# Kernel tuning notes

Hardware: AMD Instinct MI355X
Metric: run time of the kernel (lower is better)

## Reference

```python
import jax, jax.numpy as jnp
import numpy as np

B, C, H, W = 32, 48, 64, 128
K = 5  # conv kernel size (1x5 / 5x1)


def _conv1d(x, w, b):
    # x: [B, C, L]; w: [O, I, K]; b: [O]. 'same' conv (pad 2) along L.
    y = jax.lax.conv_general_dilated(x, w, window_strides=(1,), padding=[(2, 2)],
                                     dimension_numbers=("NCH", "OIH", "NCH"))
    return y + b[None, :, None]


def setup_inputs() -> dict:
    key = jax.random.key(0)
    ks = jax.random.split(key, 7)
    s = 0.02  # small init so the 64/128-step linear recurrences stay bounded
    return {
        "x": jax.random.normal(ks[0], (B, C, H, W), dtype=jnp.float32),
        "down_w": jax.random.normal(ks[1], (C, C, K), dtype=jnp.float32) * s,
        "down_b": jax.random.normal(ks[2], (C,), dtype=jnp.float32) * s,
        "right_w": jax.random.normal(ks[3], (C, C, K), dtype=jnp.float32) * s,
        "right_b": jax.random.normal(ks[4], (C,), dtype=jnp.float32) * s,
        "left_w": jax.random.normal(ks[5], (C, C, K), dtype=jnp.float32) * s,
        "left_b": jax.random.normal(ks[6], (C,), dtype=jnp.float32) * s,
    }


def reference(x, down_w, down_b, right_w, right_b, left_w, left_b):
    Bb, Cc, Hh, Ww = x.shape

    def step(w, b):
        def f(carry, inp):
            nxt = inp + _conv1d(carry, w, b)
            return nxt, nxt
        return f

    # --- down pass: d[0]=x[0]; d[t]=x[t]+down_conv(d[t-1]) ---
    xs = jnp.moveaxis(x, 2, 0)                       # [H, B, C, W]
    d0 = xs[0]
    _, d_rest = jax.lax.scan(step(down_w, down_b), d0, xs[1:])
    D = jnp.concatenate([d0[None], d_rest], 0)       # [H, B, C, W]

    # --- up pass: faithfully uses down_conv (source quirk) with index H-3-t
    # u[0]=D[H-1]; u[k]=D[H-2-k]+down_conv(u[k-1]), k=1..H-1 (H-2-k=-1 -> D[H-1])
    seq = jnp.concatenate([D[Hh - 3::-1], D[Hh - 1:Hh]], 0)  # [H-1, B, C, W]
    u0 = D[Hh - 1]
    _, u_rest = jax.lax.scan(step(down_w, down_b), u0, seq)
    U = jnp.concatenate([u0[None], u_rest], 0)[::-1]  # U[i] = u[H-1-i]

    # --- right pass over width: r[0]=U[...,0]; r[t]=U[...,t]+right_conv(r[t-1]) ---
    ws = jnp.moveaxis(jnp.moveaxis(U, 0, 2), 3, 0)   # [W, B, C, H]
    r0 = ws[0]
    _, r_rest = jax.lax.scan(step(right_w, right_b), r0, ws[1:])
    R = jnp.concatenate([r0[None], r_rest], 0)       # [W, B, C, H]

    # --- left pass (reverse): l[0]=R[W-1]; l[k]=R[W-1-k]+left_conv(l[k-1]) ---
    l0 = R[Ww - 1]
    _, l_rest = jax.lax.scan(step(left_w, left_b), l0, R[Ww - 2::-1])
    L = jnp.concatenate([l0[None], l_rest], 0)[::-1]  # [W, B, C, H]

    return jnp.moveaxis(L, 0, 3)                     # [B, C, H, W]
```

## Files before the change

### kernel.cpp

```cpp
#include <hip/hip_runtime.h>
#include <hip/hip_bf16.h>

#define B_ 32
#define C_ 48
#define H_ 64
#define W_ 128
#define K_ 5
#define SLAB (C_*H_*W_)
#define RS 72
#define ROWS 132
#define KB 10
#define WC (W_*C_)
#define HC (H_*C_)

typedef __attribute__((ext_vector_type(8))) short short8;
typedef __attribute__((ext_vector_type(4))) float f32x4;

__device__ __forceinline__ void lbar() {
  asm volatile("s_waitcnt lgkmcnt(0)\n\ts_barrier" ::: "memory");
}

__device__ __forceinline__ unsigned short f2bf(float f) {
  union { float f; unsigned u; } v; v.f = f;
  unsigned r = v.u + 0x7fffu + ((v.u >> 16) & 1u);
  return (unsigned short)(r >> 16);
}

__device__ __forceinline__ unsigned pk2(float a, float b) {
  union { __hip_bfloat162 h; unsigned u; } z;
  z.h = __float22bfloat162_rn(float2{a, b});
  return z.u;
}

__device__ __forceinline__ void load_wA(const float* __restrict__ wgt,
                                        const float* __restrict__ bias,
                                        short8 A[3][KB], float bv[3][4],
                                        int l15, int q) {
#pragma unroll
  for (int mt = 0; mt < 3; ++mt) {
#pragma unroll
    for (int r = 0; r < 4; ++r) bv[mt][r] = bias[mt * 16 + 4 * q + r];
#pragma unroll
    for (int kb = 0; kb < KB; ++kb) {
      short8 f;
#pragma unroll
      for (int j = 0; j < 8; ++j) {
        int kp = kb * 32 + q * 8 + j, k = kp >> 6, i = kp & 63;
        f[j] = (i < C_) ? (short)f2bf(wgt[(mt * 16 + l15) * (C_ * K_) + i * K_ + k])
                        : (short)0;
      }
      A[mt][kb] = f;
    }
  }
}

template<int NTW>
__device__ __forceinline__ void load_xin(float4 xv[NTW][3], const float* __restrict__ inp,
                                         int lRS, int n0, int l15, int c0) {
#pragma unroll
  for (int nt = 0; nt < NTW; ++nt) {
    const float* p = inp + (size_t)(n0 + nt * 16 + l15) * lRS;
#pragma unroll
    for (int mt = 0; mt < 3; ++mt)
      xv[nt][mt] = *(const float4*)(p + mt * 16 + c0);
  }
}

template<int NTW>
__device__ __forceinline__ void do_step(const unsigned short* __restrict__ scr,
                                        unsigned short* __restrict__ scw,
                                        const short8 A[3][KB], const float bv[3][4],
                                        const float4 xv[NTW][3],
                                        float* __restrict__ outp,
                                        int n0, int l15, int q, int c0) {
  f32x4 acc[NTW][3];
#pragma unroll
  for (int nt = 0; nt < NTW; ++nt)
#pragma unroll
    for (int mt = 0; mt < 3; ++mt) acc[nt][mt] = (f32x4){0.f, 0.f, 0.f, 0.f};

#pragma unroll
  for (int kb = 0; kb < KB; ++kb) {
    short8 pf[NTW];
#pragma unroll
    for (int nt = 0; nt < NTW; ++nt)
      pf[nt] = *(const short8*)(scr + (size_t)(n0 + nt * 16 + l15 + (kb >> 1)) * RS
                                + (kb & 1) * 32 + q * 8);
#pragma unroll
    for (int nt = 0; nt < NTW; ++nt)
#pragma unroll
      for (int mt = 0; mt < 3; ++mt)
        acc[nt][mt] = __builtin_amdgcn_mfma_f32_16x16x32_bf16(A[mt][kb], pf[nt],
                                                              acc[nt][mt], 0, 0, 0);
  }

#pragma unroll
  for (int nt = 0; nt < NTW; ++nt) {
    const int row = n0 + nt * 16 + l15;
#pragma unroll
    for (int mt = 0; mt < 3; ++mt) {
      float4 v;
      v.x = acc[nt][mt][0] + xv[nt][mt].x + bv[mt][0];
      v.y = acc[nt][mt][1] + xv[nt][mt].y + bv[mt][1];
      v.z = acc[nt][mt][2] + xv[nt][mt].z + bv[mt][2];
      v.w = acc[nt][mt][3] + xv[nt][mt].w + bv[mt][3];
      *(float4*)(outp + (size_t)row * C_ + mt * 16 + c0) = v;
      uint2 pk; pk.x = pk2(v.x, v.y); pk.y = pk2(v.z, v.w);
      *(uint2*)(scw + (size_t)(row + 2) * RS + mt * 16 + c0) = pk;
    }
  }
  lbar();
}

template<int NTW>
__device__ __forceinline__ void init_store(unsigned short* __restrict__ scw,
                                           const float* __restrict__ inp, int lRS,
                                           float* __restrict__ outp,
                                           int n0, int l15, int q, int c0) {
  float4 xv[NTW][3];
  load_xin<NTW>(xv, inp, lRS, n0, l15, c0);
#pragma unroll
  for (int nt = 0; nt < NTW; ++nt) {
    const int row = n0 + nt * 16 + l15;
#pragma unroll
    for (int mt = 0; mt < 3; ++mt) {
      float4 v = xv[nt][mt];
      *(float4*)(outp + (size_t)row * C_ + mt * 16 + c0) = v;
      uint2 pk; pk.x = pk2(v.x, v.y); pk.y = pk2(v.z, v.w);
      *(uint2*)(scw + (size_t)(row + 2) * RS + mt * 16 + c0) = pk;
    }
  }
  lbar();
}

template<int NTW, class FIN, class FOUT>
__device__ __forceinline__ void run_pass(unsigned short* sb, int& p,
                                         const short8 A[3][KB], const float bv[3][4],
                                         int nsteps, FIN inadr, int lRS, FOUT outadr,
                                         int n0, int l15, int q, int c0) {
  float4 xa[NTW][3], xb[NTW][3];
  load_xin<NTW>(xa, inadr(1), lRS, n0, l15, c0);
  for (int s = 1; s <= nsteps; s += 2) {
    {
      int sn = (s + 1 <= nsteps) ? s + 1 : nsteps;
      load_xin<NTW>(xb, inadr(sn), lRS, n0, l15, c0);
      __builtin_amdgcn_sched_barrier(0x38F);
      do_step<NTW>(sb + (size_t)p * (ROWS * RS), sb + (size_t)(p ^ 1) * (ROWS * RS),
                   A, bv, xa, outadr(s), n0, l15, q, c0);
      p ^= 1;
    }
    if (s + 1 <= nsteps) {
      int sn = (s + 2 <= nsteps) ? s + 2 : nsteps;
      load_xin<NTW>(xa, inadr(sn), lRS, n0, l15, c0);
      __builtin_amdgcn_sched_barrier(0x38F);
      do_step<NTW>(sb + (size_t)p * (ROWS * RS), sb + (size_t)(p ^ 1) * (ROWS * RS),
                   A, bv, xb, outadr(s + 1), n0, l15, q, c0);
      p ^= 1;
    }
  }
}

__global__ __launch_bounds__(256, 1) void scnn_mfma(
    float* ws,
    const float* __restrict__ dw, const float* __restrict__ db,
    const float* __restrict__ rw, const float* __restrict__ rb,
    const float* __restrict__ lw, const float* __restrict__ lb,
    float* __restrict__ DU)
{
  __shared__ unsigned short sb[2 * ROWS * RS];
  const int tid = threadIdx.x, lane = tid & 63, wid = tid >> 6;
  const int l15 = lane & 15, q = lane >> 4, c0 = 4 * q;
  const int b = blockIdx.x;
  float* xbuf = ws + (size_t)b * SLAB;
  float* rl   = ws + (size_t)b * SLAB;
  float* du   = DU + (size_t)b * SLAB;
  const int n0w = wid * 32, n0h = wid * 16;

  short8 A[3][KB];
  float bv[3][4];
  int p = 0;

  load_wA(dw, db, A, bv, l15, q);
  { unsigned* z = (unsigned*)sb; for (int i = tid; i < ROWS * RS; i += 256) z[i] = 0u; }
  __syncthreads();
  init_store<2>(sb, xbuf, C_, du, n0w, l15, q, c0);
  run_pass<2>(sb, p, A, bv, H_ - 1,
              [&](int s) { return xbuf + (size_t)s * WC; }, C_,
              [&](int s) { return du + (size_t)s * WC; }, n0w, l15, q, c0);
  __syncthreads();

  run_pass<2>(sb, p, A, bv, H_ - 1,
              [&](int s) { int ih = (s <= H_ - 2) ? (H_ - 2 - s) : (H_ - 1);
                           return du + (size_t)ih * WC; }, C_,
              [&](int s) { return du + (size_t)(H_ - 1 - s) * WC; }, n0w, l15, q, c0);
  __syncthreads();

  load_wA(rw, rb, A, bv, l15, q);
  { unsigned* z = (unsigned*)sb; for (int i = tid; i < ROWS * RS; i += 256) z[i] = 0u; }
  __syncthreads();
  p = 0;
  init_store<1>(sb, du, WC, rl, n0h, l15, q, c0);
  run_pass<1>(sb, p, A, bv, W_ - 1,
              [&](int s) { return du + (size_t)s * C_; }, WC,
              [&](int s) { return rl + (size_t)s * HC; }, n0h, l15, q, c0);
  __syncthreads();

  load_wA(lw, lb, A, bv, l15, q);
  run_pass<1>(sb, p, A, bv, W_ - 1,
              [&](int s) { return rl + (size_t)(W_ - 1 - s) * HC; }, C_,
              [&](int s) { return rl + (size_t)(W_ - 1 - s) * HC; }, n0h, l15, q, c0);
}

__global__ __launch_bounds__(256) void xpose_chw_hwc(const float* __restrict__ x,
                                                     float* __restrict__ xT) {
  __shared__ float t[C_ * 129];
  const int bh = blockIdx.x, b = bh >> 6, h = bh & 63;
  const float* src = x + (size_t)b * SLAB + (size_t)h * W_;
  float* dst = xT + (size_t)b * SLAB + (size_t)h * (W_ * C_);
  for (int i = threadIdx.x; i < C_ * W_; i += 256) {
    int c = i >> 7, w = i & 127;
    t[c * 129 + w] = src[(size_t)c * (H_ * W_) + w];
  }
  __syncthreads();
  for (int i = threadIdx.x; i < C_ * W_; i += 256) {
    int w = i / C_, c = i - w * C_;
    dst[i] = t[c * 129 + w];
  }
}

__global__ __launch_bounds__(256) void xpose_whc_chw(const float* __restrict__ L,
                                                     float* __restrict__ out) {
  __shared__ float t[W_ * 49];
  const int bh = blockIdx.x, b = bh >> 6, h = bh & 63;
  const float* src = L + (size_t)b * SLAB + (size_t)h * C_;
  float* dst = out + (size_t)b * SLAB + (size_t)h * W_;
  for (int i = threadIdx.x; i < W_ * C_; i += 256) {
    int w = i / C_, c = i - w * C_;
    t[w * 49 + c] = src[(size_t)w * (H_ * C_) + c];
  }
  __syncthreads();
  for (int i = threadIdx.x; i < C_ * W_; i += 256) {
    int c = i >> 7, w = i & 127;
    dst[(size_t)c * (H_ * W_) + w] = t[w * 49 + c];
  }
}

extern "C" void kernel_launch(void* const* d_in, const int* in_sizes, int n_in,
                              void* d_out, int out_size, void* d_ws, size_t ws_size,
                              hipStream_t stream) {
  const float* x  = (const float*)d_in[0];
  const float* dw = (const float*)d_in[1];
  const float* db = (const float*)d_in[2];
  const float* rw = (const float*)d_in[3];
  const float* rb = (const float*)d_in[4];
  const float* lw = (const float*)d_in[5];
  const float* lb = (const float*)d_in[6];
  float* DU = (float*)d_out;
  float* WS = (float*)d_ws;

  xpose_chw_hwc<<<B_ * H_, 256, 0, stream>>>(x, WS);
  scnn_mfma<<<B_, 256, 0, stream>>>(WS, dw, db, rw, rb, lw, lb, DU);
  xpose_whc_chw<<<B_ * H_, 256, 0, stream>>>(WS, DU);
}
```

Baseline: 445.4 us.

## Run each batch recurrence on a single wavefront to remove per-step barriers

```diff
diff --git a/kernel.cpp b/kernel.cpp
--- a/kernel.cpp
+++ b/kernel.cpp
@@ -12,13 +12,10 @@
 #define KB 10
 #define WC (W_*C_)
 #define HC (H_*C_)
+#define CBUF (ROWS*RS)
 
 typedef __attribute__((ext_vector_type(8))) short short8;
 typedef __attribute__((ext_vector_type(4))) float f32x4;
-
-__device__ __forceinline__ void lbar() {
-  asm volatile("s_waitcnt lgkmcnt(0)\n\ts_barrier" ::: "memory");
-}
 
 __device__ __forceinline__ unsigned short f2bf(float f) {
   union { float f; unsigned u; } v; v.f = f;
@@ -54,161 +51,136 @@
   }
 }
 
-template<int NTW>
-__device__ __forceinline__ void load_xin(float4 xv[NTW][3], const float* __restrict__ inp,
-                                         int lRS, int n0, int l15, int c0) {
-#pragma unroll
-  for (int nt = 0; nt < NTW; ++nt) {
-    const float* p = inp + (size_t)(n0 + nt * 16 + l15) * lRS;
-#pragma unroll
-    for (int mt = 0; mt < 3; ++mt)
-      xv[nt][mt] = *(const float4*)(p + mt * 16 + c0);
-  }
-}
-
-template<int NTW>
+template<int NT>
 __device__ __forceinline__ void do_step(const unsigned short* __restrict__ scr,
                                         unsigned short* __restrict__ scw,
                                         const short8 A[3][KB], const float bv[3][4],
-                                        const float4 xv[NTW][3],
+                                        const float* __restrict__ inp, size_t lRS,
                                         float* __restrict__ outp,
-                                        int n0, int l15, int q, int c0) {
-  f32x4 acc[NTW][3];
-#pragma unroll
-  for (int nt = 0; nt < NTW; ++nt)
-#pragma unroll
-    for (int mt = 0; mt < 3; ++mt) acc[nt][mt] = (f32x4){0.f, 0.f, 0.f, 0.f};
-
-#pragma unroll
-  for (int kb = 0; kb < KB; ++kb) {
-    short8 pf[NTW];
-#pragma unroll
-    for (int nt = 0; nt < NTW; ++nt)
-      pf[nt] = *(const short8*)(scr + (size_t)(n0 + nt * 16 + l15 + (kb >> 1)) * RS
-                                + (kb & 1) * 32 + q * 8);
-#pragma unroll
-    for (int nt = 0; nt < NTW; ++nt)
+                                        int l15, int q, int c0) {
+  float4 xv[NT][3];
+#pragma unroll
+  for (int nt = 0; nt < NT; ++nt) {
+    const float* p = inp + (size_t)(nt * 16 + l15) * lRS + c0;
+#pragma unroll
+    for (int mt = 0; mt < 3; ++mt) xv[nt][mt] = *(const float4*)(p + mt * 16);
+  }
+  __builtin_amdgcn_sched_barrier(0);
+
+#pragma unroll
+  for (int g = 0; g < NT / 2; ++g) {
+    f32x4 acc[2][3];
+#pragma unroll
+    for (int u = 0; u < 2; ++u)
 #pragma unroll
       for (int mt = 0; mt < 3; ++mt)
-        acc[nt][mt] = __builtin_amdgcn_mfma_f32_16x16x32_bf16(A[mt][kb], pf[nt],
-                                                              acc[nt][mt], 0, 0, 0);
-  }
-
-#pragma unroll
-  for (int nt = 0; nt < NTW; ++nt) {
-    const int row = n0 + nt * 16 + l15;
+        acc[u][mt] = (f32x4){bv[mt][0], bv[mt][1], bv[mt][2], bv[mt][3]};
+#pragma unroll
+    for (int kb = 0; kb < KB; ++kb) {
+      short8 pf[2];
+#pragma unroll
+      for (int u = 0; u < 2; ++u)
+        pf[u] = *(const short8*)(scr
+                 + (size_t)((2 * g + u) * 16 + l15 + (kb >> 1)) * RS
+                 + (kb & 1) * 32 + q * 8);
+#pragma unroll
+      for (int u = 0; u < 2; ++u)
+#pragma unroll
+        for (int mt = 0; mt < 3; ++mt)
+          acc[u][mt] = __builtin_amdgcn_mfma_f32_16x16x32_bf16(A[mt][kb], pf[u],
+                                                               acc[u][mt], 0, 0, 0);
+    }
+#pragma unroll
+    for (int u = 0; u < 2; ++u) {
+      const int row = (2 * g + u) * 16 + l15;
+#pragma unroll
+      for (int mt = 0; mt < 3; ++mt) {
+        float4 v;
+        v.x = acc[u][mt][0] + xv[2 * g + u][mt].x;
+        v.y = acc[u][mt][1] + xv[2 * g + u][mt].y;
+        v.z = acc[u][mt][2] + xv[2 * g + u][mt].z;
+        v.w = acc[u][mt][3] + xv[2 * g + u][mt].w;
+        *(float4*)(outp + (size_t)row * C_ + mt * 16 + c0) = v;
+        uint2 pk; pk.x = pk2(v.x, v.y); pk.y = pk2(v.z, v.w);
+        *(uint2*)(scw + (size_t)(row + 2) * RS + mt * 16 + c0) = pk;
+      }
+    }
+  }
+}
+
+template<int NT>
+__device__ __forceinline__ void init_step(unsigned short* __restrict__ scw,
+                                          const float* __restrict__ inp, size_t lRS,
+                                          float* __restrict__ outp,
+                                          int l15, int q, int c0) {
+#pragma unroll
+  for (int nt = 0; nt < NT; ++nt) {
+    const int row = nt * 16 + l15;
+    const float* p = inp + (size_t)row * lRS + c0;
 #pragma unroll
     for (int mt = 0; mt < 3; ++mt) {
-      float4 v;
-      v.x = acc[nt][mt][0] + xv[nt][mt].x + bv[mt][0];
-      v.y = acc[nt][mt][1] + xv[nt][mt].y + bv[mt][1];
-      v.z = acc[nt][mt][2] + xv[nt][mt].z + bv[mt][2];
-      v.w = acc[nt][mt][3] + xv[nt][mt].w + bv[mt][3];
+      float4 v = *(const float4*)(p + mt * 16);
       *(float4*)(outp + (size_t)row * C_ + mt * 16 + c0) = v;
       uint2 pk; pk.x = pk2(v.x, v.y); pk.y = pk2(v.z, v.w);
       *(uint2*)(scw + (size_t)(row + 2) * RS + mt * 16 + c0) = pk;
     }
   }
-  lbar();
-}
-
-template<int NTW>
-__device__ __forceinline__ void init_store(unsigned short* __restrict__ scw,
-                                           const float* __restrict__ inp, int lRS,
-                                           float* __restrict__ outp,
-                                           int n0, int l15, int q, int c0) {
-  float4 xv[NTW][3];
-  load_xin<NTW>(xv, inp, lRS, n0, l15, c0);
-#pragma unroll
-  for (int nt = 0; nt < NTW; ++nt) {
-    const int row = n0 + nt * 16 + l15;
-#pragma unroll
-    for (int mt = 0; mt < 3; ++mt) {
-      float4 v = xv[nt][mt];
-      *(float4*)(outp + (size_t)row * C_ + mt * 16 + c0) = v;
-      uint2 pk; pk.x = pk2(v.x, v.y); pk.y = pk2(v.z, v.w);
-      *(uint2*)(scw + (size_t)(row + 2) * RS + mt * 16 + c0) = pk;
-    }
-  }
-  lbar();
-}
-
-template<int NTW, class FIN, class FOUT>
-__device__ __forceinline__ void run_pass(unsigned short* sb, int& p,
-                                         const short8 A[3][KB], const float bv[3][4],
-                                         int nsteps, FIN inadr, int lRS, FOUT outadr,
-                                         int n0, int l15, int q, int c0) {
-  float4 xa[NTW][3], xb[NTW][3];
-  load_xin<NTW>(xa, inadr(1), lRS, n0, l15, c0);
-  for (int s = 1; s <= nsteps; s += 2) {
-    {
-      int sn = (s + 1 <= nsteps) ? s + 1 : nsteps;
-      load_xin<NTW>(xb, inadr(sn), lRS, n0, l15, c0);
-      __builtin_amdgcn_sched_barrier(0x38F);
-      do_step<NTW>(sb + (size_t)p * (ROWS * RS), sb + (size_t)(p ^ 1) * (ROWS * RS),
-                   A, bv, xa, outadr(s), n0, l15, q, c0);
-      p ^= 1;
-    }
-    if (s + 1 <= nsteps) {
-      int sn = (s + 2 <= nsteps) ? s + 2 : nsteps;
-      load_xin<NTW>(xa, inadr(sn), lRS, n0, l15, c0);
-      __builtin_amdgcn_sched_barrier(0x38F);
-      do_step<NTW>(sb + (size_t)p * (ROWS * RS), sb + (size_t)(p ^ 1) * (ROWS * RS),
-                   A, bv, xb, outadr(s + 1), n0, l15, q, c0);
-      p ^= 1;
-    }
-  }
-}
-
-__global__ __launch_bounds__(256, 1) void scnn_mfma(
+}
+
+__global__ __launch_bounds__(64, 1) void scnn_mfma(
     float* ws,
     const float* __restrict__ dw, const float* __restrict__ db,
     const float* __restrict__ rw, const float* __restrict__ rb,
     const float* __restrict__ lw, const float* __restrict__ lb,
     float* __restrict__ DU)
 {
-  __shared__ unsigned short sb[2 * ROWS * RS];
-  const int tid = threadIdx.x, lane = tid & 63, wid = tid >> 6;
+  __shared__ unsigned short sb[2 * CBUF];
+  const int lane = threadIdx.x;
   const int l15 = lane & 15, q = lane >> 4, c0 = 4 * q;
   const int b = blockIdx.x;
   float* xbuf = ws + (size_t)b * SLAB;
   float* rl   = ws + (size_t)b * SLAB;
   float* du   = DU + (size_t)b * SLAB;
-  const int n0w = wid * 32, n0h = wid * 16;
 
   short8 A[3][KB];
   float bv[3][4];
   int p = 0;
 
   load_wA(dw, db, A, bv, l15, q);
-  { unsigned* z = (unsigned*)sb; for (int i = tid; i < ROWS * RS; i += 256) z[i] = 0u; }
-  __syncthreads();
-  init_store<2>(sb, xbuf, C_, du, n0w, l15, q, c0);
-  run_pass<2>(sb, p, A, bv, H_ - 1,
-              [&](int s) { return xbuf + (size_t)s * WC; }, C_,
-              [&](int s) { return du + (size_t)s * WC; }, n0w, l15, q, c0);
-  __syncthreads();
-
-  run_pass<2>(sb, p, A, bv, H_ - 1,
-              [&](int s) { int ih = (s <= H_ - 2) ? (H_ - 2 - s) : (H_ - 1);
-                           return du + (size_t)ih * WC; }, C_,
-              [&](int s) { return du + (size_t)(H_ - 1 - s) * WC; }, n0w, l15, q, c0);
-  __syncthreads();
+  { unsigned* z = (unsigned*)sb; for (int i = lane; i < CBUF; i += 64) z[i] = 0u; }
+  init_step<8>(sb, xbuf, (size_t)C_, du, l15, q, c0);
+  p = 0;
+  for (int s = 1; s < H_; ++s) {
+    do_step<8>(sb + (size_t)p * CBUF, sb + (size_t)(p ^ 1) * CBUF, A, bv,
+               xbuf + (size_t)s * WC, (size_t)C_, du + (size_t)s * WC, l15, q, c0);
+    p ^= 1;
+  }
+
+  for (int s = 1; s < H_; ++s) {
+    int ih = (s <= H_ - 2) ? (H_ - 2 - s) : (H_ - 1);
+    do_step<8>(sb + (size_t)p * CBUF, sb + (size_t)(p ^ 1) * CBUF, A, bv,
+               du + (size_t)ih * WC, (size_t)C_,
+               du + (size_t)(H_ - 1 - s) * WC, l15, q, c0);
+    p ^= 1;
+  }
 
   load_wA(rw, rb, A, bv, l15, q);
-  { unsigned* z = (unsigned*)sb; for (int i = tid; i < ROWS * RS; i += 256) z[i] = 0u; }
-  __syncthreads();
+  { unsigned* z = (unsigned*)sb; for (int i = lane; i < CBUF; i += 64) z[i] = 0u; }
   p = 0;
-  init_store<1>(sb, du, WC, rl, n0h, l15, q, c0);
-  run_pass<1>(sb, p, A, bv, W_ - 1,
-              [&](int s) { return du + (size_t)s * C_; }, WC,
-              [&](int s) { return rl + (size_t)s * HC; }, n0h, l15, q, c0);
-  __syncthreads();
+  init_step<4>(sb, du, (size_t)WC, rl, l15, q, c0);
+  for (int s = 1; s < W_; ++s) {
+    do_step<4>(sb + (size_t)p * CBUF, sb + (size_t)(p ^ 1) * CBUF, A, bv,
+               du + (size_t)s * C_, (size_t)WC, rl + (size_t)s * HC, l15, q, c0);
+    p ^= 1;
+  }
 
   load_wA(lw, lb, A, bv, l15, q);
-  run_pass<1>(sb, p, A, bv, W_ - 1,
-              [&](int s) { return rl + (size_t)(W_ - 1 - s) * HC; }, C_,
-              [&](int s) { return rl + (size_t)(W_ - 1 - s) * HC; }, n0h, l15, q, c0);
+  for (int s = 1; s < W_; ++s) {
+    do_step<4>(sb + (size_t)p * CBUF, sb + (size_t)(p ^ 1) * CBUF, A, bv,
+               rl + (size_t)(W_ - 1 - s) * HC, (size_t)C_,
+               rl + (size_t)(W_ - 1 - s) * HC, l15, q, c0);
+    p ^= 1;
+  }
 }
 
 __global__ __launch_bounds__(256) void xpose_chw_hwc(const float* __restrict__ x,
@@ -259,6 +231,6 @@
   float* WS = (float*)d_ws;
 
   xpose_chw_hwc<<<B_ * H_, 256, 0, stream>>>(x, WS);
-  scnn_mfma<<<B_, 256, 0, stream>>>(WS, dw, db, rw, rb, lw, lb, DU);
+  scnn_mfma<<<B_, 64, 0, stream>>>(WS, dw, db, rw, rb, lw, lb, DU);
   xpose_whc_chw<<<B_ * H_, 256, 0, stream>>>(WS, DU);
 }
```

After: 1.039 ms. 2.33x slower.

## Pack conv reduction densely to 8 MFMA k-blocks with split accumulators

Applied to the files above, without the earlier changes.

```diff
diff --git a/kernel.cpp b/kernel.cpp
--- a/kernel.cpp
+++ b/kernel.cpp
@@ -7,11 +7,12 @@
 #define W_ 128
 #define K_ 5
 #define SLAB (C_*H_*W_)
-#define RS 72
-#define ROWS 132
-#define KB 10
+#define RS 56
+#define ROWS 136
+#define CBUF (ROWS*RS)
 #define WC (W_*C_)
 #define HC (H_*C_)
+#define KBN 8
 
 typedef __attribute__((ext_vector_type(8))) short short8;
 typedef __attribute__((ext_vector_type(4))) float f32x4;
@@ -34,20 +35,22 @@
 
 __device__ __forceinline__ void load_wA(const float* __restrict__ wgt,
                                         const float* __restrict__ bias,
-                                        short8 A[3][KB], float bv[3][4],
-                                        int l15, int q) {
+                                        short8 A[3][KBN], f32x4 bv[3],
+                                        int l15, int q8, int c0) {
 #pragma unroll
   for (int mt = 0; mt < 3; ++mt) {
 #pragma unroll
-    for (int r = 0; r < 4; ++r) bv[mt][r] = bias[mt * 16 + 4 * q + r];
-#pragma unroll
-    for (int kb = 0; kb < KB; ++kb) {
+    for (int r = 0; r < 4; ++r) bv[mt][r] = bias[mt * 16 + c0 + r];
+#pragma unroll
+    for (int kb = 0; kb < KBN; ++kb) {
       short8 f;
 #pragma unroll
       for (int j = 0; j < 8; ++j) {
-        int kp = kb * 32 + q * 8 + j, k = kp >> 6, i = kp & 63;
-        f[j] = (i < C_) ? (short)f2bf(wgt[(mt * 16 + l15) * (C_ * K_) + i * K_ + k])
-                        : (short)0;
+        int kp = kb * 32 + q8 + j;
+        int k = kp / 48, i = kp - 48 * k;
+        f[j] = (kp < 240)
+             ? (short)f2bf(wgt[(mt * 16 + l15) * (C_ * K_) + i * K_ + k])
+             : (short)0;
       }
       A[mt][kb] = f;
     }
@@ -56,42 +59,43 @@
 
 template<int NTW>
 __device__ __forceinline__ void load_xin(float4 xv[NTW][3], const float* __restrict__ inp,
-                                         int lRS, int n0, int l15, int c0) {
+                                         size_t lRS, int n0, int l15, int c0) {
 #pragma unroll
   for (int nt = 0; nt < NTW; ++nt) {
-    const float* p = inp + (size_t)(n0 + nt * 16 + l15) * lRS;
-#pragma unroll
-    for (int mt = 0; mt < 3; ++mt)
-      xv[nt][mt] = *(const float4*)(p + mt * 16 + c0);
-  }
-}
-
-template<int NTW>
+    const float* p = inp + (size_t)(n0 + nt * 16 + l15) * lRS + c0;
+#pragma unroll
+    for (int mt = 0; mt < 3; ++mt) xv[nt][mt] = *(const float4*)(p + mt * 16);
+  }
+}
+
+template<int NTW, int SPL>
 __device__ __forceinline__ void do_step(const unsigned short* __restrict__ scr,
                                         unsigned short* __restrict__ scw,
-                                        const short8 A[3][KB], const float bv[3][4],
-                                        const float4 xv[NTW][3],
+                                        const short8 A[3][KBN], const f32x4 bv[3],
+                                        const float4 xv[NTW][3], const int off_r[KBN],
                                         float* __restrict__ outp,
-                                        int n0, int l15, int q, int c0) {
-  f32x4 acc[NTW][3];
-#pragma unroll
-  for (int nt = 0; nt < NTW; ++nt)
-#pragma unroll
-    for (int mt = 0; mt < 3; ++mt) acc[nt][mt] = (f32x4){0.f, 0.f, 0.f, 0.f};
-
-#pragma unroll
-  for (int kb = 0; kb < KB; ++kb) {
+                                        int n0, int l15, int c0) {
+  f32x4 acc[SPL][NTW][3];
+#pragma unroll
+  for (int s = 0; s < SPL; ++s)
+#pragma unroll
+    for (int nt = 0; nt < NTW; ++nt)
+#pragma unroll
+      for (int mt = 0; mt < 3; ++mt)
+        acc[s][nt][mt] = (s == 0) ? bv[mt] : (f32x4){0.f, 0.f, 0.f, 0.f};
+
+#pragma unroll
+  for (int kb = 0; kb < KBN; ++kb) {
     short8 pf[NTW];
 #pragma unroll
     for (int nt = 0; nt < NTW; ++nt)
-      pf[nt] = *(const short8*)(scr + (size_t)(n0 + nt * 16 + l15 + (kb >> 1)) * RS
-                                + (kb & 1) * 32 + q * 8);
+      pf[nt] = *(const short8*)(scr + (size_t)(n0 + nt * 16) * RS + off_r[kb]);
 #pragma unroll
     for (int nt = 0; nt < NTW; ++nt)
 #pragma unroll
       for (int mt = 0; mt < 3; ++mt)
-        acc[nt][mt] = __builtin_amdgcn_mfma_f32_16x16x32_bf16(A[mt][kb], pf[nt],
-                                                              acc[nt][mt], 0, 0, 0);
+        acc[kb % SPL][nt][mt] = __builtin_amdgcn_mfma_f32_16x16x32_bf16(
+            A[mt][kb], pf[nt], acc[kb % SPL][nt][mt], 0, 0, 0);
   }
 
 #pragma unroll
@@ -99,11 +103,14 @@
     const int row = n0 + nt * 16 + l15;
 #pragma unroll
     for (int mt = 0; mt < 3; ++mt) {
+      f32x4 a = acc[0][nt][mt];
+#pragma unroll
+      for (int s = 1; s < SPL; ++s)
+#pragma unroll
+        for (int r = 0; r < 4; ++r) a[r] += acc[s][nt][mt][r];
       float4 v;
-      v.x = acc[nt][mt][0] + xv[nt][mt].x + bv[mt][0];
-      v.y = acc[nt][mt][1] + xv[nt][mt].y + bv[mt][1];
-      v.z = acc[nt][mt][2] + xv[nt][mt].z + bv[mt][2];
-      v.w = acc[nt][mt][3] + xv[nt][mt].w + bv[mt][3];
+      v.x = a[0] + xv[nt][mt].x; v.y = a[1] + xv[nt][mt].y;
+      v.z = a[2] + xv[nt][mt].z; v.w = a[3] + xv[nt][mt].w;
       *(float4*)(outp + (size_t)row * C_ + mt * 16 + c0) = v;
       uint2 pk; pk.x = pk2(v.x, v.y); pk.y = pk2(v.z, v.w);
       *(uint2*)(scw + (size_t)(row + 2) * RS + mt * 16 + c0) = pk;
@@ -114,9 +121,9 @@
 
 template<int NTW>
 __device__ __forceinline__ void init_store(unsigned short* __restrict__ scw,
-                                           const float* __restrict__ inp, int lRS,
+                                           const float* __restrict__ inp, size_t lRS,
                                            float* __restrict__ outp,
-                                           int n0, int l15, int q, int c0) {
+                                           int n0, int l15, int c0) {
   float4 xv[NTW][3];
   load_xin<NTW>(xv, inp, lRS, n0, l15, c0);
 #pragma unroll
@@ -133,11 +140,12 @@
   lbar();
 }
 
-template<int NTW, class FIN, class FOUT>
+template<int NTW, int SPL, class FIN, class FOUT>
 __device__ __forceinline__ void run_pass(unsigned short* sb, int& p,
-                                         const short8 A[3][KB], const float bv[3][4],
-                                         int nsteps, FIN inadr, int lRS, FOUT outadr,
-                                         int n0, int l15, int q, int c0) {
+                                         const short8 A[3][KBN], const f32x4 bv[3],
+                                         const int off_r[KBN],
+                                         int nsteps, FIN inadr, size_t lRS, FOUT outadr,
+                                         int n0, int l15, int c0) {
   float4 xa[NTW][3], xb[NTW][3];
   load_xin<NTW>(xa, inadr(1), lRS, n0, l15, c0);
   for (int s = 1; s <= nsteps; s += 2) {
@@ -145,16 +153,16 @@
       int sn = (s + 1 <= nsteps) ? s + 1 : nsteps;
       load_xin<NTW>(xb, inadr(sn), lRS, n0, l15, c0);
       __builtin_amdgcn_sched_barrier(0x38F);
-      do_step<NTW>(sb + (size_t)p * (ROWS * RS), sb + (size_t)(p ^ 1) * (ROWS * RS),
-                   A, bv, xa, outadr(s), n0, l15, q, c0);
+      do_step<NTW, SPL>(sb + (size_t)p * CBUF, sb + (size_t)(p ^ 1) * CBUF,
+                        A, bv, xa, off_r, outadr(s), n0, l15, c0);
       p ^= 1;
     }
     if (s + 1 <= nsteps) {
       int sn = (s + 2 <= nsteps) ? s + 2 : nsteps;
       load_xin<NTW>(xa, inadr(sn), lRS, n0, l15, c0);
       __builtin_amdgcn_sched_barrier(0x38F);
-      do_step<NTW>(sb + (size_t)p * (ROWS * RS), sb + (size_t)(p ^ 1) * (ROWS * RS),
-                   A, bv, xb, outadr(s + 1), n0, l15, q, c0);
+      do_step<NTW, SPL>(sb + (size_t)p * CBUF, sb + (size_t)(p ^ 1) * CBUF,
+                        A, bv, xb, off_r, outadr(s + 1), n0, l15, c0);
       p ^= 1;
     }
   }
@@ -167,48 +175,56 @@
     const float* __restrict__ lw, const float* __restrict__ lb,
     float* __restrict__ DU)
 {
-  __shared__ unsigned short sb[2 * ROWS * RS];
+  __shared__ unsigned short sb[2 * CBUF];
   const int tid = threadIdx.x, lane = tid & 63, wid = tid >> 6;
-  const int l15 = lane & 15, q = lane >> 4, c0 = 4 * q;
+  const int l15 = lane & 15, q = lane >> 4, q8 = q * 8, c0 = 4 * q;
   const int b = blockIdx.x;
   float* xbuf = ws + (size_t)b * SLAB;
   float* rl   = ws + (size_t)b * SLAB;
   float* du   = DU + (size_t)b * SLAB;
   const int n0w = wid * 32, n0h = wid * 16;
 
-  short8 A[3][KB];
-  float bv[3][4];
+  int off_r[KBN];
+#pragma unroll
+  for (int kb = 0; kb < KBN; ++kb) {
+    int s = kb * 32 + q8;
+    int k = s / 48, i0 = s - 48 * k;
+    off_r[kb] = (l15 + k) * RS + i0;
+  }
+
+  short8 A[3][KBN];
+  f32x4 bv[3];
   int p = 0;
 
-  load_wA(dw, db, A, bv, l15, q);
-  { unsigned* z = (unsigned*)sb; for (int i = tid; i < ROWS * RS; i += 256) z[i] = 0u; }
-  __syncthreads();
-  init_store<2>(sb, xbuf, C_, du, n0w, l15, q, c0);
-  run_pass<2>(sb, p, A, bv, H_ - 1,
-              [&](int s) { return xbuf + (size_t)s * WC; }, C_,
-              [&](int s) { return du + (size_t)s * WC; }, n0w, l15, q, c0);
-  __syncthreads();
-
-  run_pass<2>(sb, p, A, bv, H_ - 1,
-              [&](int s) { int ih = (s <= H_ - 2) ? (H_ - 2 - s) : (H_ - 1);
-                           return du + (size_t)ih * WC; }, C_,
-              [&](int s) { return du + (size_t)(H_ - 1 - s) * WC; }, n0w, l15, q, c0);
-  __syncthreads();
-
-  load_wA(rw, rb, A, bv, l15, q);
-  { unsigned* z = (unsigned*)sb; for (int i = tid; i < ROWS * RS; i += 256) z[i] = 0u; }
+  load_wA(dw, db, A, bv, l15, q8, c0);
+  { unsigned* z = (unsigned*)sb; for (int i = tid; i < CBUF; i += 256) z[i] = 0u; }
+  __syncthreads();
+  init_store<2>(sb, xbuf, (size_t)C_, du, n0w, l15, c0);
+  run_pass<2, 2>(sb, p, A, bv, off_r, H_ - 1,
+                 [&](int s) { return xbuf + (size_t)s * WC; }, (size_t)C_,
+                 [&](int s) { return du + (size_t)s * WC; }, n0w, l15, c0);
+  __syncthreads();
+
+  run_pass<2, 2>(sb, p, A, bv, off_r, H_ - 1,
+                 [&](int s) { int ih = (s <= H_ - 2) ? (H_ - 2 - s) : (H_ - 1);
+                              return du + (size_t)ih * WC; }, (size_t)C_,
+                 [&](int s) { return du + (size_t)(H_ - 1 - s) * WC; }, n0w, l15, c0);
+  __syncthreads();
+
+  load_wA(rw, rb, A, bv, l15, q8, c0);
+  { unsigned* z = (unsigned*)sb; for (int i = tid; i < CBUF; i += 256) z[i] = 0u; }
   __syncthreads();
   p = 0;
-  init_store<1>(sb, du, WC, rl, n0h, l15, q, c0);
-  run_pass<1>(sb, p, A, bv, W_ - 1,
-              [&](int s) { return du + (size_t)s * C_; }, WC,
-              [&](int s) { return rl + (size_t)s * HC; }, n0h, l15, q, c0);
-  __syncthreads();
-
-  load_wA(lw, lb, A, bv, l15, q);
-  run_pass<1>(sb, p, A, bv, W_ - 1,
-              [&](int s) { return rl + (size_t)(W_ - 1 - s) * HC; }, C_,
-              [&](int s) { return rl + (size_t)(W_ - 1 - s) * HC; }, n0h, l15, q, c0);
+  init_store<1>(sb, du, (size_t)WC, rl, n0h, l15, c0);
+  run_pass<1, 4>(sb, p, A, bv, off_r, W_ - 1,
+                 [&](int s) { return du + (size_t)s * C_; }, (size_t)WC,
+                 [&](int s) { return rl + (size_t)s * HC; }, n0h, l15, c0);
+  __syncthreads();
+
+  load_wA(lw, lb, A, bv, l15, q8, c0);
+  run_pass<1, 4>(sb, p, A, bv, off_r, W_ - 1,
+                 [&](int s) { return rl + (size_t)(W_ - 1 - s) * HC; }, (size_t)C_,
+                 [&](int s) { return rl + (size_t)(W_ - 1 - s) * HC; }, n0h, l15, c0);
 }
 
 __global__ __launch_bounds__(256) void xpose_chw_hwc(const float* __restrict__ x,
```

Measured after the change: 408.8 us. -8.2%, faster.
